# Performance work log

Measured on AMD Instinct MI355X. Metric: run time of the kernel, lower is better.

The kernel has to match this reference:

```python
import jax, jax.numpy as jnp
import numpy as np

N_LAYER = 4
N_HEAD = 16
N_EMBD = 1024
BLOCK = 1024
VOCAB = 100
TRANS = 16          # obs_dim + action_dim + 2 = 11 + 3 + 2
OBS_DIM = 11
ACT_DIM = 3
B, T = 2, 1024
VTOT = VOCAB * TRANS + 1  # token embedding rows
LN_EPS = 1e-5


def _layernorm(x, w, b):
    mu = jnp.mean(x, axis=-1, keepdims=True)
    var = jnp.var(x, axis=-1, keepdims=True)
    return (x - mu) * jax.lax.rsqrt(var + LN_EPS) * w + b


def _build_mask(t):
    # causal tril with every (joined_dim-1 mod joined_dim) column zeroed
    jd = OBS_DIM + ACT_DIM + 2  # 16
    m = jnp.tril(jnp.ones((t, t), dtype=bool))
    cols = jnp.arange(t)
    m = m & ((cols % jd) != (jd - 1))[None, :]
    return m  # [T, T] bool, True = keep


def setup_inputs() -> dict:
    key = jax.random.key(0)
    ks = jax.random.split(key, 24)
    C, L, F4 = N_EMBD, N_LAYER, 4 * N_EMBD
    g = lambda k, s: jax.random.normal(k, s, dtype=jnp.float32) * 0.02
    return {
        "tokens": jax.random.randint(ks[0], (B, T), 0, VTOT),
        "tok_emb": g(ks[1], (VTOT, C)),
        "pos_emb": g(ks[2], (1, BLOCK, C)),
        "Wq": g(ks[3], (L, C, C)), "bq": jnp.zeros((L, C), jnp.float32),
        "Wk": g(ks[4], (L, C, C)), "bk": jnp.zeros((L, C), jnp.float32),
        "Wv": g(ks[5], (L, C, C)), "bv": jnp.zeros((L, C), jnp.float32),
        "Wp": g(ks[6], (L, C, C)), "bp": jnp.zeros((L, C), jnp.float32),
        "ln1w": jnp.ones((L, C), jnp.float32), "ln1b": jnp.zeros((L, C), jnp.float32),
        "ln2w": jnp.ones((L, C), jnp.float32), "ln2b": jnp.zeros((L, C), jnp.float32),
        "W1": g(ks[7], (L, C, F4)), "b1": jnp.zeros((L, F4), jnp.float32),
        "W2": g(ks[8], (L, F4, C)), "b2": jnp.zeros((L, C), jnp.float32),
        "lnfw": jnp.ones((C,), jnp.float32), "lnfb": jnp.zeros((C,), jnp.float32),
        "head_w": g(ks[9], (TRANS, VOCAB + 1, C)),
    }


def _forward(tokens, tok_emb, pos_emb, Wq, bq, Wk, bk, Wv, bv, Wp, bp,
             ln1w, ln1b, ln2w, ln2b, W1, b1, W2, b2, lnfw, lnfb, head_w):
    b, t = tokens.shape
    C, H = N_EMBD, N_HEAD
    D = C // H
    scale = 1.0 / np.sqrt(D)
    mask = _build_mask(t)[None, None]  # [1,1,T,T]

    x = tok_emb[tokens] + pos_emb[:, :t, :]  # [B,T,C]
    for i in range(N_LAYER):
        h = _layernorm(x, ln1w[i], ln1b[i])
        q = (h @ Wq[i] + bq[i]).reshape(b, t, H, D).transpose(0, 2, 1, 3)
        k = (h @ Wk[i] + bk[i]).reshape(b, t, H, D).transpose(0, 2, 1, 3)
        v = (h @ Wv[i] + bv[i]).reshape(b, t, H, D).transpose(0, 2, 1, 3)
        att = jnp.einsum('bhtd,bhsd->bhts', q, k) * scale  # attn_bias=None => +0
        att = jnp.where(mask, att, -jnp.inf)
        att = jax.nn.softmax(att, axis=-1)
        y = jnp.einsum('bhts,bhsd->bhtd', att, v)
        y = y.transpose(0, 2, 1, 3).reshape(b, t, C)
        x = x + (y @ Wp[i] + bp[i])
        h2 = _layernorm(x, ln2w[i], ln2b[i])
        x = x + (jax.nn.gelu(h2 @ W1[i] + b1[i], approximate=False) @ W2[i] + b2[i])

    x = _layernorm(x, lnfw, lnfb)
    # pad_to_full_observation + EinLinear head
    n_pad = (TRANS - t % TRANS) % TRANS
    if n_pad:
        x = jnp.concatenate([x, jnp.zeros((b, n_pad, C), x.dtype)], axis=1)
    x_pad = x.reshape(-1, TRANS, C)                    # [b*n_states, TRANS, C]
    logits = jnp.einsum('eoi,bei->beo', head_w, x_pad)  # EinLinear, bias=False
    logits = logits.reshape(b, t + n_pad, VOCAB + 1)[:, :t]
    return logits


def reference(tokens, tok_emb, pos_emb, Wq, bq, Wk, bk, Wv, bv, Wp, bp,
              ln1w, ln1b, ln2w, ln2b, W1, b1, W2, b2, lnfw, lnfb, head_w):
    return _forward(tokens, tok_emb, pos_emb, Wq, bq, Wk, bk, Wv, bv, Wp, bp,
                    ln1w, ln1b, ln2w, ln2b, W1, b1, W2, b2, lnfw, lnfb, head_w)
```

## Files before the change

### kernel.cpp

```cpp
#include <hip/hip_runtime.h>
#include <hip/hip_bf16.h>
#include <math.h>

typedef unsigned short u16;
typedef __attribute__((ext_vector_type(8))) short short8;
typedef __attribute__((ext_vector_type(4))) float f32x4;

#define CDIM 1024
#define TDIM 1024
#define NROWS 2048
#define HEADS 16
#define HD 64
#define F4 4096

__device__ __forceinline__ u16 f2bf(float f) {
    union { float f; unsigned u; } v; v.f = f;
    unsigned r = v.u + 0x7fffu + ((v.u >> 16) & 1u);
    return (u16)(r >> 16);
}

__device__ __forceinline__ void gload_lds16(const void* g, void* lds) {
    __builtin_amdgcn_global_load_lds(
        (const __attribute__((address_space(1))) unsigned int*)g,
        (__attribute__((address_space(3))) unsigned int*)lds,
        16, 0, 0);
}

__device__ __forceinline__ void tile_map(int& bx, int& by, int& bz)
{
    const int gx = gridDim.x, gy = gridDim.y;
    const int fid = blockIdx.x + gx * (blockIdx.y + gy * blockIdx.z);
    const int nwg = gx * gy * gridDim.z;
    const int q = nwg >> 3, r = nwg & 7;
    const int xcd = fid & 7, t = fid >> 3;
    const int n = ((xcd < r) ? xcd * (q + 1) : r * (q + 1) + (xcd - r) * q) + t;
    const int nxy = gx * gy;
    bz = n / nxy;
    const int xy = n - bz * nxy;
    const int per_group = gx << 3;
    const int grp = xy / per_group;
    const int in = xy - grp * per_group;
    const int y0 = grp << 3;
    const int rem = gy - y0;
    const int gh = rem < 8 ? rem : 8;
    by = y0 + (in % gh);
    bx = in / gh;
}

__global__ __launch_bounds__(256)
void embed_k(const int* __restrict__ tok, const float* __restrict__ te,
             const float* __restrict__ pe, float* __restrict__ X)
{
    const int row = blockIdx.x;
    const int t = row & (TDIM - 1);
    const int tk = tok[row];
    const int c = threadIdx.x * 4;
    float4 a = *reinterpret_cast<const float4*>(te + (size_t)tk * CDIM + c);
    float4 b = *reinterpret_cast<const float4*>(pe + (size_t)t * CDIM + c);
    a.x += b.x; a.y += b.y; a.z += b.z; a.w += b.w;
    *reinterpret_cast<float4*>(X + (size_t)row * CDIM + c) = a;
}

template<bool BF16OUT>
__global__ __launch_bounds__(256)
void ln_k(const float* __restrict__ X, const float* __restrict__ g,
          const float* __restrict__ be, void* __restrict__ outp)
{
    __shared__ float red[4], red2[4];
    const int row = blockIdx.x, tid = threadIdx.x;
    const float* xr = X + (size_t)row * CDIM;
    const int c = tid * 4;
    float4 xv = *reinterpret_cast<const float4*>(xr + c);
    float s  = xv.x + xv.y + xv.z + xv.w;
    float s2 = xv.x*xv.x + xv.y*xv.y + xv.z*xv.z + xv.w*xv.w;
    #pragma unroll
    for (int off = 32; off; off >>= 1) {
        s  += __shfl_xor(s, off);
        s2 += __shfl_xor(s2, off);
    }
    if ((tid & 63) == 0) { red[tid >> 6] = s; red2[tid >> 6] = s2; }
    __syncthreads();
    const float ts  = red[0] + red[1] + red[2] + red[3];
    const float ts2 = red2[0] + red2[1] + red2[2] + red2[3];
    const float mu  = ts * (1.0f / CDIM);
    const float var = ts2 * (1.0f / CDIM) - mu * mu;
    const float rs  = rsqrtf(var + 1e-5f);
    float4 gv = *reinterpret_cast<const float4*>(g + c);
    float4 bv = *reinterpret_cast<const float4*>(be + c);
    float o0 = (xv.x - mu) * rs * gv.x + bv.x;
    float o1 = (xv.y - mu) * rs * gv.y + bv.y;
    float o2 = (xv.z - mu) * rs * gv.z + bv.z;
    float o3 = (xv.w - mu) * rs * gv.w + bv.w;
    if (BF16OUT) {
        u16 tmp[4] = { f2bf(o0), f2bf(o1), f2bf(o2), f2bf(o3) };
        u16* o = (u16*)outp + (size_t)row * CDIM + c;
        *reinterpret_cast<uint2*>(o) = *reinterpret_cast<const uint2*>(tmp);
    } else {
        float4 ov = { o0, o1, o2, o3 };
        *reinterpret_cast<float4*>((float*)outp + (size_t)row * CDIM + c) = ov;
    }
}

__global__ __launch_bounds__(256)
void convT_k(const float* __restrict__ W, u16* __restrict__ Wt,
             const int K, const int N)
{
    __shared__ u16 s[64][72];
    const int k0 = blockIdx.y * 64, n0 = blockIdx.x * 64;
    const int tr = threadIdx.x >> 4, tc = (threadIdx.x & 15) * 4;
    #pragma unroll
    for (int i = 0; i < 4; ++i) {
        int r = tr + i * 16;
        float4 w = *reinterpret_cast<const float4*>(W + (size_t)(k0 + r) * N + n0 + tc);
        s[r][tc + 0] = f2bf(w.x); s[r][tc + 1] = f2bf(w.y);
        s[r][tc + 2] = f2bf(w.z); s[r][tc + 3] = f2bf(w.w);
    }
    __syncthreads();
    #pragma unroll
    for (int i = 0; i < 4; ++i) {
        int n = tr + i * 16;
        u16 tmp[4];
        #pragma unroll
        for (int e = 0; e < 4; ++e) tmp[e] = s[tc + e][n];
        *reinterpret_cast<uint2*>(Wt + (size_t)(n0 + n) * K + k0 + tc) =
            *reinterpret_cast<const uint2*>(tmp);
    }
}

__global__ __launch_bounds__(256)
void pack_bias_k(const float* __restrict__ a, const float* __restrict__ b,
                 const float* __restrict__ c, float* __restrict__ o)
{
    const int i = threadIdx.x * 4;
    const float* s = blockIdx.x == 0 ? a : blockIdx.x == 1 ? b : c;
    *reinterpret_cast<float4*>(o + (size_t)blockIdx.x * 1024 + i) =
        *reinterpret_cast<const float4*>(s + i);
}

template<int EPI>
__global__ __launch_bounds__(256, 2)
void gemm_bt(const u16* __restrict__ A, const u16* __restrict__ Bt,
             const float* __restrict__ bias, u16* __restrict__ outb,
             float* __restrict__ resid, u16* __restrict__ vtout,
             const int N, const int K, const int KCH)
{
    __shared__ __align__(16) u16 sA[2][2][128 * 32];
    __shared__ __align__(16) u16 sB[2][2][128 * 32];
    const int tid = threadIdx.x;
    const int lane = tid & 63, wv = tid >> 6;
    int bx, by, bz;
    tile_map(bx, by, bz);
    const int m0 = by * 128, n0 = bx * 128;
    const int kbeg = bz * KCH, kend = kbeg + KCH;
    const int fr = lane & 15, fq = lane >> 4;
    const int wm = wv & 1, wn = wv >> 1;
    const int srow = lane >> 2, schunk = (lane & 3) * 8;
    f32x4 acc[4][4] = {};

    auto stage = [&](int k0, int buf) {
        #pragma unroll
        for (int kk = 0; kk < 2; ++kk)
            #pragma unroll
            for (int i = 0; i < 2; ++i) {
                const int reg = i * 4 + wv;
                gload_lds16(A  + (size_t)(m0 + reg * 16 + srow) * K + k0 + kk * 32 + schunk,
                            &sA[buf][kk][reg * 512]);
                gload_lds16(Bt + (size_t)(n0 + reg * 16 + srow) * K + k0 + kk * 32 + schunk,
                            &sB[buf][kk][reg * 512]);
            }
    };

    stage(kbeg, 0);
    int cur = 0;
    for (int k0 = kbeg; k0 < kend; k0 += 64) {
        __syncthreads();
        if (k0 + 64 < kend) stage(k0 + 64, cur ^ 1);
        #pragma unroll
        for (int kk = 0; kk < 2; ++kk) {
            short8 af[4], bf[4];
            #pragma unroll
            for (int mi = 0; mi < 4; ++mi)
                af[mi] = *reinterpret_cast<const short8*>(
                    &sA[cur][kk][(wm * 64 + mi * 16 + fr) * 32 + fq * 8]);
            #pragma unroll
            for (int nj = 0; nj < 4; ++nj)
                bf[nj] = *reinterpret_cast<const short8*>(
                    &sB[cur][kk][(wn * 64 + nj * 16 + fr) * 32 + fq * 8]);
            #pragma unroll
            for (int mi = 0; mi < 4; ++mi)
                #pragma unroll
                for (int nj = 0; nj < 4; ++nj)
                    acc[mi][nj] = __builtin_amdgcn_mfma_f32_16x16x32_bf16(af[mi], bf[nj], acc[mi][nj], 0, 0, 0);
        }
        cur ^= 1;
    }

    #pragma unroll
    for (int nj = 0; nj < 4; ++nj) {
        const int col = n0 + wn * 64 + nj * 16 + fr;
        const float bias_v = (EPI == 2 && bz != 0) ? 0.0f : bias[col];
        #pragma unroll
        for (int mi = 0; mi < 4; ++mi) {
            const int rowb = m0 + wm * 64 + mi * 16 + fq * 4;
            if (EPI == 0 && vtout != nullptr && col >= 2048) {
                const int bidx = rowb >> 10, t = rowb & 1023, hd = col - 2048;
                u16 t4[4];
                #pragma unroll
                for (int r = 0; r < 4; ++r) t4[r] = f2bf(acc[mi][nj][r] + bias_v);
                *reinterpret_cast<uint2*>(
                    vtout + ((size_t)(bidx * 16 + (hd >> 6)) * 64 + (hd & 63)) * 1024 + t) =
                    *reinterpret_cast<const uint2*>(t4);
            } else {
                #pragma unroll
                for (int r = 0; r < 4; ++r) {
                    const int row = rowb + r;
                    float cv = acc[mi][nj][r] + bias_v;
                    if (EPI == 0) {
                        outb[(size_t)row * N + col] = f2bf(cv);
                    } else if (EPI == 1) {
                        float gl = 0.5f * cv * (1.0f + erff(cv * 0.70710678118654752f));
                        outb[(size_t)row * N + col] = f2bf(gl);
                    } else {
                        atomicAdd(&resid[(size_t)row * N + col], cv);
                    }
                }
            }
        }
    }
}

__global__ __launch_bounds__(256)
void attn_k(const u16* __restrict__ QKV, const u16* __restrict__ VT,
            u16* __restrict__ Y)
{
    __shared__ __align__(16) u16 sQ[64][72];
    __shared__ __align__(16) u16 sK[2][64][72];
    __shared__ __align__(16) u16 sV[2][64][72];
    __shared__ __align__(16) u16 sP[64][72];
    const int tid = threadIdx.x, lane = tid & 63, wv = tid >> 6;
    const int fr = lane & 15, fq = lane >> 4;
    int bx, by, bz;
    tile_map(bx, by, bz);
    const int qt = gridDim.x - 1 - bx;
    const int h = by, b = bz, q0 = qt * 64;
    const u16* Qb = QKV + (size_t)b * TDIM * 3072 + h * HD;
    const u16* Vb = VT + ((size_t)(b * HEADS + h) * HD) * TDIM;
    const int r0 = tid >> 3, c0 = (tid & 7) * 8;

    #pragma unroll
    for (int i = 0; i < 2; ++i) {
        const int r = r0 + i * 32;
        *reinterpret_cast<uint4*>(&sQ[r][c0]) =
            *reinterpret_cast<const uint4*>(Qb + (size_t)(q0 + r) * 3072 + c0);
        *reinterpret_cast<uint4*>(&sK[0][r][c0]) =
            *reinterpret_cast<const uint4*>(Qb + 1024 + (size_t)r * 3072 + c0);
        *reinterpret_cast<uint4*>(&sV[0][r][c0]) =
            *reinterpret_cast<const uint4*>(Vb + (size_t)r * TDIM + c0);
    }
    __syncthreads();

    short8 ones;
    #pragma unroll
    for (int e = 0; e < 8; ++e) ones[e] = (short)0x3F80;

    short8 aQ0 = *reinterpret_cast<const short8*>(&sQ[wv * 16 + fr][fq * 8]);
    short8 aQ1 = *reinterpret_cast<const short8*>(&sQ[wv * 16 + fr][32 + fq * 8]);
    f32x4 o[4] = {};
    f32x4 osum = {};

    for (int st = 0; st <= qt; ++st) {
        const int cur = st & 1, s0 = st * 64;
        const bool pf = st < qt;
        uint4 pk[2], pv[2];
        if (pf) {
            #pragma unroll
            for (int i = 0; i < 2; ++i) {
                const int r = r0 + i * 32;
                pk[i] = *reinterpret_cast<const uint4*>(Qb + 1024 + (size_t)(s0 + 64 + r) * 3072 + c0);
                pv[i] = *reinterpret_cast<const uint4*>(Vb + (size_t)r * TDIM + s0 + 64 + c0);
            }
        }
        f32x4 sacc[4] = {};
        #pragma unroll
        for (int j = 0; j < 4; ++j) {
            short8 b0 = *reinterpret_cast<const short8*>(&sK[cur][j * 16 + fr][fq * 8]);
            sacc[j] = __builtin_amdgcn_mfma_f32_16x16x32_bf16(aQ0, b0, sacc[j], 0, 0, 0);
            short8 b1 = *reinterpret_cast<const short8*>(&sK[cur][j * 16 + fr][32 + fq * 8]);
            sacc[j] = __builtin_amdgcn_mfma_f32_16x16x32_bf16(aQ1, b1, sacc[j], 0, 0, 0);
        }
        #pragma unroll
        for (int j = 0; j < 4; ++j)
            #pragma unroll
            for (int r = 0; r < 4; ++r) {
                const int qrow = q0 + wv * 16 + fq * 4 + r;
                const int scol = s0 + j * 16 + fr;
                const bool keep = (scol <= qrow) && ((scol & 15) != 15);
                const float p = keep ? __expf(sacc[j][r] * 0.125f) : 0.0f;
                sP[wv * 16 + fq * 4 + r][j * 16 + fr] = f2bf(p);
            }
        short8 aP0 = *reinterpret_cast<const short8*>(&sP[wv * 16 + fr][fq * 8]);
        short8 aP1 = *reinterpret_cast<const short8*>(&sP[wv * 16 + fr][32 + fq * 8]);
        #pragma unroll
        for (int j = 0; j < 4; ++j) {
            short8 b0 = *reinterpret_cast<const short8*>(&sV[cur][j * 16 + fr][fq * 8]);
            o[j] = __builtin_amdgcn_mfma_f32_16x16x32_bf16(aP0, b0, o[j], 0, 0, 0);
            short8 b1 = *reinterpret_cast<const short8*>(&sV[cur][j * 16 + fr][32 + fq * 8]);
            o[j] = __builtin_amdgcn_mfma_f32_16x16x32_bf16(aP1, b1, o[j], 0, 0, 0);
        }
        osum = __builtin_amdgcn_mfma_f32_16x16x32_bf16(aP0, ones, osum, 0, 0, 0);
        osum = __builtin_amdgcn_mfma_f32_16x16x32_bf16(aP1, ones, osum, 0, 0, 0);
        if (pf) {
            #pragma unroll
            for (int i = 0; i < 2; ++i) {
                const int r = r0 + i * 32;
                *reinterpret_cast<uint4*>(&sK[cur ^ 1][r][c0]) = pk[i];
                *reinterpret_cast<uint4*>(&sV[cur ^ 1][r][c0]) = pv[i];
            }
        }
        __syncthreads();
    }

    float rcp[4];
    #pragma unroll
    for (int r = 0; r < 4; ++r) rcp[r] = 1.0f / osum[r];
    const size_t ybase = ((size_t)b * TDIM + q0) * CDIM + h * HD;
    #pragma unroll
    for (int j = 0; j < 4; ++j)
        #pragma unroll
        for (int r = 0; r < 4; ++r) {
            const int row = wv * 16 + fq * 4 + r, col = j * 16 + fr;
            Y[ybase + (size_t)row * CDIM + col] = f2bf(o[j][r] * rcp[r]);
        }
}

__global__ __launch_bounds__(256)
void head_k(const float* __restrict__ Xf, const float* __restrict__ HW,
             float* __restrict__ out)
{
    const int row = blockIdx.x;
    const int e = row & 15;
    const float* xr = Xf + (size_t)row * CDIM;
    const float* wbase = HW + (size_t)e * 101 * CDIM;
    const int lane = threadIdx.x & 63, wv = threadIdx.x >> 6;
    for (int o = wv; o < 101; o += 4) {
        const float* wr = wbase + (size_t)o * CDIM;
        float s = 0.0f;
        #pragma unroll
        for (int i = 0; i < CDIM / 64; ++i)
            s += xr[lane + i * 64] * wr[lane + i * 64];
        #pragma unroll
        for (int off = 32; off; off >>= 1) s += __shfl_xor(s, off);
        if (lane == 0) out[(size_t)row * 101 + o] = s;
    }
}

extern "C" void kernel_launch(void* const* d_in, const int* in_sizes, int n_in,
                              void* d_out, int out_size, void* d_ws, size_t ws_size,
                              hipStream_t stream)
{
    const int*   tokens = (const int*)  d_in[0];
    const float* tok_emb= (const float*)d_in[1];
    const float* pos_emb= (const float*)d_in[2];
    const float* Wq = (const float*)d_in[3];
    const float* bq = (const float*)d_in[4];
    const float* Wk = (const float*)d_in[5];
    const float* bk = (const float*)d_in[6];
    const float* Wv = (const float*)d_in[7];
    const float* bv = (const float*)d_in[8];
    const float* Wp = (const float*)d_in[9];
    const float* bp = (const float*)d_in[10];
    const float* ln1w = (const float*)d_in[11];
    const float* ln1b = (const float*)d_in[12];
    const float* ln2w = (const float*)d_in[13];
    const float* ln2b = (const float*)d_in[14];
    const float* W1 = (const float*)d_in[15];
    const float* b1 = (const float*)d_in[16];
    const float* W2 = (const float*)d_in[17];
    const float* b2 = (const float*)d_in[18];
    const float* lnfw = (const float*)d_in[19];
    const float* lnfb = (const float*)d_in[20];
    const float* head_w = (const float*)d_in[21];
    float* out = (float*)d_out;

    char* ws = (char*)d_ws;
    float* x    = (float*)(ws);
    u16*   hbuf = (u16*)  (ws + (8u  << 20));
    u16*   yb   = (u16*)  (ws + (8u  << 20));
    u16*   qkv  = (u16*)  (ws + (12u << 20));
    u16*   vt   = (u16*)  (ws + (24u << 20));
    u16*   mid  = (u16*)  (ws + (12u << 20));
    float* hf   = (float*)(ws + (12u << 20));
    u16*   wbuf = (u16*)  (ws + (28u << 20));
    float* bbuf = (float*)(ws + (36u << 20));

    embed_k<<<NROWS, 256, 0, stream>>>(tokens, tok_emb, pos_emb, x);

    for (int l = 0; l < 4; ++l) {
        const size_t wo = (size_t)l * CDIM * CDIM;
        convT_k<<<dim3(16, 16), 256, 0, stream>>>(Wq + wo, wbuf + 0u * CDIM * CDIM, CDIM, CDIM);
        convT_k<<<dim3(16, 16), 256, 0, stream>>>(Wk + wo, wbuf + 1u * CDIM * CDIM, CDIM, CDIM);
        convT_k<<<dim3(16, 16), 256, 0, stream>>>(Wv + wo, wbuf + 2u * CDIM * CDIM, CDIM, CDIM);
        pack_bias_k<<<3, 256, 0, stream>>>(bq + l * CDIM, bk + l * CDIM, bv + l * CDIM, bbuf);

        ln_k<true><<<NROWS, 256, 0, stream>>>(x, ln1w + l * CDIM, ln1b + l * CDIM, hbuf);
        gemm_bt<0><<<dim3(24, 16, 1), 256, 0, stream>>>(hbuf, wbuf, bbuf, qkv, nullptr, vt, 3072, CDIM, CDIM);
        attn_k<<<dim3(16, HEADS, 2), 256, 0, stream>>>(qkv, vt, yb);

        convT_k<<<dim3(16, 16), 256, 0, stream>>>(Wp + wo, wbuf, CDIM, CDIM);
        gemm_bt<2><<<dim3(8, 16, 2), 256, 0, stream>>>(yb, wbuf, bp + l * CDIM, nullptr, x, nullptr, CDIM, CDIM, 512);

        ln_k<true><<<NROWS, 256, 0, stream>>>(x, ln2w + l * CDIM, ln2b + l * CDIM, hbuf);
        convT_k<<<dim3(64, 16), 256, 0, stream>>>(W1 + (size_t)l * CDIM * F4, wbuf, CDIM, F4);
        gemm_bt<1><<<dim3(32, 16, 1), 256, 0, stream>>>(hbuf, wbuf, b1 + l * F4, mid, nullptr, nullptr, F4, CDIM, CDIM);
        convT_k<<<dim3(16, 64), 256, 0, stream>>>(W2 + (size_t)l * F4 * CDIM, wbuf, F4, CDIM);
        gemm_bt<2><<<dim3(8, 16, 4), 256, 0, stream>>>(mid, wbuf, b2 + l * CDIM, nullptr, x, nullptr, CDIM, F4, CDIM);
    }

    ln_k<false><<<NROWS, 256, 0, stream>>>(x, lnfw, lnfb, hf);
    head_k<<<NROWS, 256, 0, stream>>>(hf, head_w, out);
}
```

Measured before the change: 1.060 ms.

## Replace split-K atomic residual adds with partial buffers reduced inside LayerNorm

After: 984.7 us. 7.1% less time.

```diff
diff --git a/kernel.cpp b/kernel.cpp
--- a/kernel.cpp
+++ b/kernel.cpp
@@ -71,6 +71,52 @@
     const float* xr = X + (size_t)row * CDIM;
     const int c = tid * 4;
     float4 xv = *reinterpret_cast<const float4*>(xr + c);
+    float s  = xv.x + xv.y + xv.z + xv.w;
+    float s2 = xv.x*xv.x + xv.y*xv.y + xv.z*xv.z + xv.w*xv.w;
+    #pragma unroll
+    for (int off = 32; off; off >>= 1) {
+        s  += __shfl_xor(s, off);
+        s2 += __shfl_xor(s2, off);
+    }
+    if ((tid & 63) == 0) { red[tid >> 6] = s; red2[tid >> 6] = s2; }
+    __syncthreads();
+    const float ts  = red[0] + red[1] + red[2] + red[3];
+    const float ts2 = red2[0] + red2[1] + red2[2] + red2[3];
+    const float mu  = ts * (1.0f / CDIM);
+    const float var = ts2 * (1.0f / CDIM) - mu * mu;
+    const float rs  = rsqrtf(var + 1e-5f);
+    float4 gv = *reinterpret_cast<const float4*>(g + c);
+    float4 bv = *reinterpret_cast<const float4*>(be + c);
+    float o0 = (xv.x - mu) * rs * gv.x + bv.x;
+    float o1 = (xv.y - mu) * rs * gv.y + bv.y;
+    float o2 = (xv.z - mu) * rs * gv.z + bv.z;
+    float o3 = (xv.w - mu) * rs * gv.w + bv.w;
+    if (BF16OUT) {
+        u16 tmp[4] = { f2bf(o0), f2bf(o1), f2bf(o2), f2bf(o3) };
+        u16* o = (u16*)outp + (size_t)row * CDIM + c;
+        *reinterpret_cast<uint2*>(o) = *reinterpret_cast<const uint2*>(tmp);
+    } else {
+        float4 ov = { o0, o1, o2, o3 };
+        *reinterpret_cast<float4*>((float*)outp + (size_t)row * CDIM + c) = ov;
+    }
+}
+
+template<bool BF16OUT, int NZ>
+__global__ __launch_bounds__(256)
+void ln_red_k(float* __restrict__ X, const float* __restrict__ P,
+              const float* __restrict__ g, const float* __restrict__ be,
+              void* __restrict__ outp)
+{
+    __shared__ float red[4], red2[4];
+    const int row = blockIdx.x, tid = threadIdx.x;
+    const int c = tid * 4;
+    float4 xv = *reinterpret_cast<const float4*>(X + (size_t)row * CDIM + c);
+    #pragma unroll
+    for (int z = 0; z < NZ; ++z) {
+        float4 pv = *reinterpret_cast<const float4*>(P + ((size_t)z * NROWS + row) * CDIM + c);
+        xv.x += pv.x; xv.y += pv.y; xv.z += pv.z; xv.w += pv.w;
+    }
+    *reinterpret_cast<float4*>(X + (size_t)row * CDIM + c) = xv;
     float s  = xv.x + xv.y + xv.z + xv.w;
     float s2 = xv.x*xv.x + xv.y*xv.y + xv.z*xv.z + xv.w*xv.w;
     #pragma unroll
@@ -221,7 +267,7 @@
                         float gl = 0.5f * cv * (1.0f + erff(cv * 0.70710678118654752f));
                         outb[(size_t)row * N + col] = f2bf(gl);
                     } else {
-                        atomicAdd(&resid[(size_t)row * N + col], cv);
+                        resid[((size_t)bz * NROWS + row) * N + col] = cv;
                     }
                 }
             }
@@ -391,7 +437,8 @@
     u16*   mid  = (u16*)  (ws + (12u << 20));
     float* hf   = (float*)(ws + (12u << 20));
     u16*   wbuf = (u16*)  (ws + (28u << 20));
-    float* bbuf = (float*)(ws + (36u << 20));
+    float* pbuf = (float*)(ws + (36u << 20));
+    float* bbuf = (float*)(ws + (68u << 20));
 
     embed_k<<<NROWS, 256, 0, stream>>>(tokens, tok_emb, pos_emb, x);
 
@@ -402,20 +449,23 @@
         convT_k<<<dim3(16, 16), 256, 0, stream>>>(Wv + wo, wbuf + 2u * CDIM * CDIM, CDIM, CDIM);
         pack_bias_k<<<3, 256, 0, stream>>>(bq + l * CDIM, bk + l * CDIM, bv + l * CDIM, bbuf);
 
-        ln_k<true><<<NROWS, 256, 0, stream>>>(x, ln1w + l * CDIM, ln1b + l * CDIM, hbuf);
+        if (l == 0)
+            ln_k<true><<<NROWS, 256, 0, stream>>>(x, ln1w, ln1b, hbuf);
+        else
+            ln_red_k<true, 4><<<NROWS, 256, 0, stream>>>(x, pbuf, ln1w + l * CDIM, ln1b + l * CDIM, hbuf);
         gemm_bt<0><<<dim3(24, 16, 1), 256, 0, stream>>>(hbuf, wbuf, bbuf, qkv, nullptr, vt, 3072, CDIM, CDIM);
         attn_k<<<dim3(16, HEADS, 2), 256, 0, stream>>>(qkv, vt, yb);
 
         convT_k<<<dim3(16, 16), 256, 0, stream>>>(Wp + wo, wbuf, CDIM, CDIM);
-        gemm_bt<2><<<dim3(8, 16, 2), 256, 0, stream>>>(yb, wbuf, bp + l * CDIM, nullptr, x, nullptr, CDIM, CDIM, 512);
-
-        ln_k<true><<<NROWS, 256, 0, stream>>>(x, ln2w + l * CDIM, ln2b + l * CDIM, hbuf);
+        gemm_bt<2><<<dim3(8, 16, 2), 256, 0, stream>>>(yb, wbuf, bp + l * CDIM, nullptr, pbuf, nullptr, CDIM, CDIM, 512);
+
+        ln_red_k<true, 2><<<NROWS, 256, 0, stream>>>(x, pbuf, ln2w + l * CDIM, ln2b + l * CDIM, hbuf);
         convT_k<<<dim3(64, 16), 256, 0, stream>>>(W1 + (size_t)l * CDIM * F4, wbuf, CDIM, F4);
         gemm_bt<1><<<dim3(32, 16, 1), 256, 0, stream>>>(hbuf, wbuf, b1 + l * F4, mid, nullptr, nullptr, F4, CDIM, CDIM);
         convT_k<<<dim3(16, 64), 256, 0, stream>>>(W2 + (size_t)l * F4 * CDIM, wbuf, F4, CDIM);
-        gemm_bt<2><<<dim3(8, 16, 4), 256, 0, stream>>>(mid, wbuf, b2 + l * CDIM, nullptr, x, nullptr, CDIM, F4, CDIM);
-    }
-
-    ln_k<false><<<NROWS, 256, 0, stream>>>(x, lnfw, lnfb, hf);
+        gemm_bt<2><<<dim3(8, 16, 4), 256, 0, stream>>>(mid, wbuf, b2 + l * CDIM, nullptr, pbuf, nullptr, CDIM, F4, CDIM);
+    }
+
+    ln_red_k<false, 4><<<NROWS, 256, 0, stream>>>(x, pbuf, lnfw, lnfb, hf);
     head_k<<<NROWS, 256, 0, stream>>>(hf, head_w, out);
 }
```
